# Performance work log

Measured on AMD Instinct MI355X. Metric: run time of the kernel, lower is better.

## Reference

```python
import jax, jax.numpy as jnp
import numpy as np

BETA = 0.25  # commitment weight (legacy=True branch)


def setup_inputs() -> dict:
    key = jax.random.key(0)
    k1, k2 = jax.random.split(key)
    B, C, H, W = 32, 256, 32, 32
    N_E, E_DIM = 1024, 256
    z = jax.random.normal(k1, (B, C, H, W), dtype=jnp.float32)
    # original init: uniform(-1/n_e, 1/n_e)
    emb = jax.random.uniform(k2, (N_E, E_DIM), dtype=jnp.float32,
                             minval=-1.0 / N_E, maxval=1.0 / N_E)
    return {"z": z, "emb": emb}


def reference(z, emb):
    B, C, H, W = z.shape
    sg = jax.lax.stop_gradient
    zt = jnp.transpose(z, (0, 2, 3, 1))            # b h w c
    zf = zt.reshape(-1, C)                          # (N, e_dim)
    # ||z||^2 + ||e||^2 - 2 z e^T  -> (N, n_e)
    d = (jnp.sum(zf * zf, axis=1, keepdims=True)
         + jnp.sum(emb * emb, axis=1)
         - 2.0 * jnp.einsum('nd,kd->nk', zf, emb))
    idx = jnp.argmin(d, axis=1)                     # (N,)
    z_q = emb[idx].reshape(zt.shape)                # b h w c
    # legacy=True loss
    loss = (jnp.mean((sg(z_q) - zt) ** 2)
            + BETA * jnp.mean((z_q - sg(zt)) ** 2))
    # straight-through estimator
    z_q_st = zt + sg(z_q - zt)
    z_q_out = jnp.transpose(z_q_st, (0, 3, 1, 2))   # b c h w
    z_indices = idx.reshape(B, 1, H, W)
    return z_q_out, loss, z_indices
```

## Files before the change

kernel.cpp:

```cpp
#include <hip/hip_runtime.h>


#define WS_B 0
#define WS_A 1024
#define WS_PV 132096
#define WS_E1 656384
#define WS_E2 787456
#define WS_LIST 918528
#define WS_CNT 951296
#define WS_Z1T 951304
#define WS_FUSED_BYTES ((size_t)(WS_Z1T + 8388608) * 4)

#define DDIM 256
#define LOSS_OFF 8388608
#define IDX_OFF 8388609
#define Z2T_OFF 8388608
#define REFINE_THR 8e-5f

typedef __attribute__((ext_vector_type(8))) short bf16x8;
typedef __attribute__((ext_vector_type(4))) float f32x4;
typedef __attribute__((ext_vector_type(8))) ushort u16x8;

__device__ __forceinline__ ushort bf16_rne(float x) {
  unsigned u = __float_as_uint(x);
  return (ushort)((u + 0x7FFFu + ((u >> 16) & 1u)) >> 16);
}
__device__ __forceinline__ float bf16f(ushort h) {
  return __uint_as_float(((unsigned)h) << 16);
}
__device__ __forceinline__ void gld16(void* l, const void* g) {
  __builtin_amdgcn_global_load_lds(
      (const __attribute__((address_space(1))) unsigned int*)g,
      (__attribute__((address_space(3))) unsigned int*)l, 16, 0, 0);
}

__global__ __launch_bounds__(256) void k_prep(const float* __restrict__ z,
                                              const float* __restrict__ emb,
                                              ushort* __restrict__ zt,
                                              float* __restrict__ ws,
                                              float* __restrict__ out) {
  __shared__ float lt[64][132];
  __shared__ float sq[128];
  const int tid = threadIdx.x;
  if (blockIdx.x >= 1024) {
    const int k = (blockIdx.x - 1024) * 256 + tid;
    if (k == 0) { out[LOSS_OFF] = 0.0f; ((int*)ws)[WS_CNT] = 0; }
    const int ct = k >> 8, n = k & 255;
    const float* er = emb + k * DDIM;
    ushort* e1t = (ushort*)(ws + WS_E1);
    ushort* e2t = (ushort*)(ws + WS_E2);
    float bsum = 0.f;
    for (int s = 0; s < 8; ++s) {
#pragma unroll
      for (int kq = 0; kq < 4; ++kq) {
        const float4 v0 = *(const float4*)(er + s * 32 + kq * 8);
        const float4 v1 = *(const float4*)(er + s * 32 + kq * 8 + 4);
        const float v[8] = {v0.x, v0.y, v0.z, v0.w, v1.x, v1.y, v1.z, v1.w};
        u16x8 h, l;
#pragma unroll
        for (int j = 0; j < 8; ++j) {
          bsum = fmaf(v[j], v[j], bsum);
          h[j] = bf16_rne(v[j]);
          l[j] = bf16_rne(v[j] - bf16f(h[j]));
        }
        const int off = ct * 65536 + s * 8192 + kq * 2048 + n * 8;
        *(u16x8*)(e1t + off) = h;
        *(u16x8*)(e2t + off) = l;
      }
    }
    ws[WS_B + k] = bsum;
    return;
  }
  const int rt = blockIdx.x >> 2;
  const int qp = blockIdx.x & 3;
  const int b = rt >> 3;
  const int hw0 = (rt & 7) << 7;
  ushort* z1t = zt;
  ushort* z2t = zt + Z2T_OFF;
  const int m = tid & 127, half = tid >> 7;
  const int lc = tid >> 2, lq = tid & 3;
  float as[4] = {0.f, 0.f, 0.f, 0.f};
  {
    const float* src = z + b * 262144 + ((qp << 6) + lc) * 1024 + hw0 + (lq << 5);
#pragma unroll
    for (int i = 0; i < 8; ++i)
      *(float4*)&lt[lc][(lq << 5) + (i << 2)] = *(const float4*)(src + (i << 2));
    __syncthreads();
    const int s = (qp << 1) + half;
#pragma unroll
    for (int kq = 0; kq < 4; ++kq) {
      u16x8 h, l;
#pragma unroll
      for (int j = 0; j < 8; ++j) {
        const float v = lt[(half << 5) + (kq << 3) + j][m];
        as[j & 3] = fmaf(v, v, as[j & 3]);
        h[j] = bf16_rne(v);
        l[j] = bf16_rne(v - bf16f(h[j]));
      }
      const int off = rt * 32768 + ((s << 2) + kq) * 1024 + (m << 3);
      *(u16x8*)(z1t + off) = h;
      *(u16x8*)(z2t + off) = l;
    }
    __syncthreads();
  }
  const float asum = (as[0] + as[1]) + (as[2] + as[3]);
  if (half) sq[m] = asum;
  __syncthreads();
  if (!half) ws[WS_A + qp * 32768 + rt * 128 + m] = asum + sq[m];
}

__global__ __launch_bounds__(512, 4) void k_score(const ushort* __restrict__ zt,
                                                  const float* __restrict__ emb,
                                                  float* out,
                                                  float* __restrict__ ws,
                                                  int fused) {
  __shared__ __align__(16) char smem[33312];
  ushort* zl = (ushort*)smem;
  float* Bs = (float*)(smem + 16384);
  float* pvs = (float*)(smem + 20480);
  float* sm2 = (float*)(smem + 33024);
  int* idxs = (int*)(smem + 33056);
  const int tid = threadIdx.x;
  const int bid = blockIdx.x;
  const int rt = ((bid >> 4) << 3) | (bid & 7);
  const int mh = ((bid >> 3) & 1) << 6;
  const int row0 = (rt << 7) + mh;
  const ushort* z1t = zt;
  const ushort* z2t = zt + Z2T_OFF;
  const ushort* e1t = (const ushort*)(ws + WS_E1);
  const ushort* e2t = (const ushort*)(ws + WS_E2);
  const int w = tid >> 6, L = tid & 63;
  const int l15 = L & 15, kq = L >> 4;
  const int wr = w >> 2, wc = w & 3;

  Bs[tid] = ws[WS_B + tid];
  Bs[tid + 512] = ws[WS_B + tid + 512];
  float Av[2][4];
#pragma unroll
  for (int mi = 0; mi < 2; ++mi) {
    const int base = row0 + (wr << 5) + (mi << 4) + (kq << 2);
    const float4 a0 = *(const float4*)(ws + WS_A + base);
    const float4 a1 = *(const float4*)(ws + WS_A + 32768 + base);
    const float4 a2 = *(const float4*)(ws + WS_A + 65536 + base);
    const float4 a3 = *(const float4*)(ws + WS_A + 98304 + base);
    Av[mi][0] = (a0.x + a1.x) + (a2.x + a3.x);
    Av[mi][1] = (a0.y + a1.y) + (a2.y + a3.y);
    Av[mi][2] = (a0.z + a1.z) + (a2.z + a3.z);
    Av[mi][3] = (a0.w + a1.w) + (a2.w + a3.w);
  }
  asm volatile("s_waitcnt vmcnt(0)" ::: "memory");
  __builtin_amdgcn_sched_barrier(0);
  __syncthreads();

  const ushort* zsrc = (w < 4 ? z1t : z2t) + rt * 32768 + ((w & 3) << 10)
                       + (mh << 3) + (L << 3);
  ushort* zdst0 = zl + ((w & 3) << 9) + ((w >> 2) << 11);
  auto stage = [&](int q, int bf) {
    gld16(zdst0 + (bf << 12), zsrc + ((q & 7) << 12));
  };
  const int ebase_th = (kq << 11) + (((wc << 6) + l15) << 3);

  f32x4 acc[2][4];
  float v1[2][4], v2[2][4];
  int i1[2][4];
#pragma unroll
  for (int mi = 0; mi < 2; ++mi)
#pragma unroll
    for (int r = 0; r < 4; ++r) {
      acc[mi][r] = (f32x4){0.f, 0.f, 0.f, 0.f};
      v1[mi][r] = 3.0e38f; v2[mi][r] = 3.0e38f; i1[mi][r] = 0;
    }

  stage(0, 0);
  stage(1, 1);

  auto body = [&](int q, int cur, bool last) {
    if (!last) asm volatile("s_waitcnt vmcnt(1)" ::: "memory");
    else       asm volatile("s_waitcnt vmcnt(0)" ::: "memory");
    __builtin_amdgcn_sched_barrier(0);
    __builtin_amdgcn_s_barrier();
    __builtin_amdgcn_sched_barrier(0);
    const ushort* lb = zl + (cur << 12);
    bf16x8 a1[2], a2[2], b1[4], b2[4];
#pragma unroll
    for (int mi = 0; mi < 2; ++mi) {
      const int off = (kq << 9) + (((wr << 5) + (mi << 4) + l15) << 3);
      a1[mi] = *(const bf16x8*)&lb[off];
      a2[mi] = *(const bf16x8*)&lb[2048 + off];
    }
    asm volatile("s_waitcnt lgkmcnt(0)" ::: "memory");
    __builtin_amdgcn_sched_barrier(0);
    __builtin_amdgcn_s_barrier();
    __builtin_amdgcn_sched_barrier(0);
    {
      const int ct = q >> 3, s = q & 7;
      const ushort* e1p = e1t + (ct << 16) + (s << 13) + ebase_th;
      const ushort* e2p = e2t + (ct << 16) + (s << 13) + ebase_th;
#pragma unroll
      for (int nj = 0; nj < 4; ++nj) {
        b1[nj] = *(const bf16x8*)(e1p + (nj << 7));
        b2[nj] = *(const bf16x8*)(e2p + (nj << 7));
      }
    }
    if (q < 30) stage(q + 2, cur);
    __builtin_amdgcn_s_setprio(1);
#pragma unroll
    for (int mi = 0; mi < 2; ++mi)
#pragma unroll
      for (int nj = 0; nj < 4; ++nj) {
        acc[mi][nj] = __builtin_amdgcn_mfma_f32_16x16x32_bf16(a2[mi], b1[nj], acc[mi][nj], 0, 0, 0);
        acc[mi][nj] = __builtin_amdgcn_mfma_f32_16x16x32_bf16(a1[mi], b2[nj], acc[mi][nj], 0, 0, 0);
        acc[mi][nj] = __builtin_amdgcn_mfma_f32_16x16x32_bf16(a1[mi], b1[nj], acc[mi][nj], 0, 0, 0);
      }
    __builtin_amdgcn_s_setprio(0);
    if ((q & 7) == 7) {
      const int ct = q >> 3;
      float bb[4];
#pragma unroll
      for (int nj = 0; nj < 4; ++nj)
        bb[nj] = Bs[(ct << 8) + (wc << 6) + (nj << 4) + l15];
      float cm[2][4];
#pragma unroll
      for (int mi = 0; mi < 2; ++mi)
#pragma unroll
        for (int r = 0; r < 4; ++r) cm[mi][r] = 3.0e38f;
#pragma unroll
      for (int mi = 0; mi < 2; ++mi)
#pragma unroll
        for (int nj = 0; nj < 4; ++nj) {
          const int kg = (ct << 8) + (wc << 6) + (nj << 4) + l15;
#pragma unroll
          for (int r = 0; r < 4; ++r) {
            const float sc = fmaf(-2.0f, acc[mi][nj][r], Av[mi][r] + bb[nj]);
            if (sc < v1[mi][r]) { v2[mi][r] = v1[mi][r]; v1[mi][r] = sc; i1[mi][r] = kg; }
            else if (sc < v2[mi][r]) v2[mi][r] = sc;
            cm[mi][r] = fminf(cm[mi][r], sc);
          }
          acc[mi][nj] = (f32x4){0.f, 0.f, 0.f, 0.f};
        }
#pragma unroll
      for (int mi = 0; mi < 2; ++mi)
#pragma unroll
        for (int r = 0; r < 4; ++r) {
          float cv = cm[mi][r];
#pragma unroll
          for (int o = 1; o < 16; o <<= 1) cv = fminf(cv, __shfl_xor(cv, o));
          if (l15 == 0) {
            const int rowl = (wr << 5) + (mi << 4) + (kq << 2) + r;
            pvs[((ct << 2) | wc) * 64 + rowl] = cv;
          }
        }
    }
  };

  for (int q = 0; q < 31; ++q) body(q, q & 1, false);
  body(31, 1, true);

#pragma unroll
  for (int mi = 0; mi < 2; ++mi)
#pragma unroll
    for (int r = 0; r < 4; ++r) {
      float a = v1[mi][r], bb = v2[mi][r];
      int ii = i1[mi][r];
#pragma unroll
      for (int o = 1; o < 16; o <<= 1) {
        const float oa = __shfl_xor(a, o);
        const float ob = __shfl_xor(bb, o);
        const int oi = __shfl_xor(ii, o);
        bb = fminf(fminf(bb, ob), fmaxf(a, oa));
        if (oa < a || (oa == a && oi < ii)) { a = oa; ii = oi; }
      }
      v1[mi][r] = a; v2[mi][r] = bb; i1[mi][r] = ii;
    }

  __syncthreads();
  for (int i = tid; i < 1024; i += 512) {
    const int c = i >> 6, rl = i & 63;
    ws[WS_PV + (c << 15) + row0 + rl] = pvs[i];
  }
  float* red = (float*)smem;
  if (l15 == 0) {
#pragma unroll
    for (int mi = 0; mi < 2; ++mi)
#pragma unroll
      for (int r = 0; r < 4; ++r) {
        const int rl = (wr << 5) + (mi << 4) + (kq << 2) + r;
        const int b3 = (wc * 64 + rl) * 3;
        red[b3] = v1[mi][r];
        red[b3 + 1] = v2[mi][r];
        red[b3 + 2] = (float)i1[mi][r];
      }
  }
  __syncthreads();
  float losss = 0.f;
  if (tid < 64) {
    float fv1 = 3.0e38f, fv2 = 3.0e38f;
    int fi = 0;
#pragma unroll
    for (int c = 0; c < 4; ++c) {
      const int b3 = (c * 64 + tid) * 3;
      const float a1 = red[b3], a2 = red[b3 + 1];
      const int ai = (int)red[b3 + 2];
      if (a1 < fv1 || (a1 == fv1 && ai < fi)) { fv2 = fminf(fv1, a2); fv1 = a1; fi = ai; }
      else fv2 = fminf(fv2, a1);
    }
    const int row = row0 + tid;
    out[IDX_OFF + row] = (float)fi;
    idxs[tid] = fi;
    if (fv2 - fv1 < REFINE_THR) {
      const int slot = atomicAdd((int*)ws + WS_CNT, 1);
      ((int*)ws)[WS_LIST + slot] = row;
    }
    losss = fv1;
  }
#pragma unroll
  for (int o = 32; o; o >>= 1) losss += __shfl_down(losss, o);
  if ((tid & 63) == 0) sm2[tid >> 6] = losss;
  __syncthreads();
  if (tid == 0) {
    float t = 0.f;
#pragma unroll
    for (int i = 0; i < 8; ++i) t += sm2[i];
    atomicAdd(out + LOSS_OFF, t * (1.25f / 8388608.0f));
  }

  if (fused) {
    float* lt2 = (float*)smem;
    const int b = row0 >> 10;
    const int hw0 = row0 & 1023;
    for (int ch = 0; ch < 2; ++ch) {
      __syncthreads();
      {
        const int r = tid >> 3, seg = tid & 7;
        const float* er = emb + idxs[r] * DDIM + (ch << 7);
        float* dst = lt2 + r * 129;
#pragma unroll
        for (int i = 0; i < 4; ++i) {
          const int c = (seg << 2) + (i << 5);
          const float4 v = *(const float4*)(er + c);
          dst[c] = v.x; dst[c + 1] = v.y; dst[c + 2] = v.z; dst[c + 3] = v.w;
        }
      }
      __syncthreads();
      {
        const int c = tid >> 2;
        const int r0 = (tid & 3) << 4;
        float* dsto = out + b * 262144 + ((ch << 7) + c) * 1024 + hw0 + r0;
#pragma unroll
        for (int i = 0; i < 16; i += 4) {
          float4 v;
          v.x = lt2[(r0 + i + 0) * 129 + c];
          v.y = lt2[(r0 + i + 1) * 129 + c];
          v.z = lt2[(r0 + i + 2) * 129 + c];
          v.w = lt2[(r0 + i + 3) * 129 + c];
          *(float4*)(dsto + i) = v;
        }
      }
    }
  }
}

__global__ __launch_bounds__(256) void k_refine(const float* __restrict__ z,
                                                const float* __restrict__ emb,
                                                const float* __restrict__ ws,
                                                float* __restrict__ out,
                                                int fused) {
  __shared__ float zs[4][256];
  const int tid = threadIdx.x;
  const int w = tid >> 6, L = tid & 63;
  const int wg = blockIdx.x * 4 + w;
  const int cnt = ((const int*)ws)[WS_CNT];
  for (int e = wg; e < cnt; e += 1024) {
    const int row = ((const int*)ws)[WS_LIST + e];
    const int b = row >> 10, hw = row & 1023;
#pragma unroll
    for (int q = 0; q < 4; ++q)
      zs[w][(q << 6) + L] = z[b * 262144 + (((q << 6) + L) << 10) + hw];
    asm volatile("s_waitcnt lgkmcnt(0)" ::: "memory");
    float v1c = (L < 16) ? ws[WS_PV + (L << 15) + row] : 3.0e38f;
    float v1 = v1c;
#pragma unroll
    for (int o = 1; o < 64; o <<= 1) v1 = fminf(v1, __shfl_xor(v1, o));
    const float A = (ws[WS_A + row] + ws[WS_A + 32768 + row]) +
                    (ws[WS_A + 65536 + row] + ws[WS_A + 98304 + row]);
    float bv = 3.0e38f;
    int bk = 0;
    for (int tc = 0; tc < 16; ++tc) {
      const float bc = __shfl(v1c, tc);
      if (bc <= v1 + REFINE_THR) {
        const int k = (tc << 6) + L;
        const float* er = emb + k * DDIM;
        float s = 0.f;
        for (int d = 0; d < DDIM; ++d) s = fmaf(zs[w][d], er[d], s);
        const float sc = fmaf(-2.0f, s, A + ws[WS_B + k]);
        if (sc < bv) { bv = sc; bk = k; }
      }
    }
#pragma unroll
    for (int o = 1; o < 64; o <<= 1) {
      const float ov = __shfl_xor(bv, o);
      const int ok = __shfl_xor(bk, o);
      if (ov < bv || (ov == bv && ok < bk)) { bv = ov; bk = ok; }
    }
    if (L == 0) out[IDX_OFF + row] = (float)bk;
    if (fused) {
#pragma unroll
      for (int ci = 0; ci < 4; ++ci) {
        const int c = (ci << 6) + L;
        out[b * 262144 + c * 1024 + hw] = emb[bk * DDIM + c];
      }
    }
  }
}

__global__ __launch_bounds__(256) void k_gather(const float* __restrict__ emb,
                                                float* __restrict__ out) {
  const int tid = threadIdx.x;
  const int e0 = (blockIdx.x * 256 + tid) * 16;
  const int b = e0 >> 18;
  const int c = (e0 >> 10) & 255;
  const int n0 = (b << 10) + (e0 & 1023);
#pragma unroll
  for (int g = 0; g < 4; ++g) {
    float q[4];
#pragma unroll
    for (int j = 0; j < 4; ++j) {
      const int id = (int)(out[IDX_OFF + n0 + g * 4 + j] + 0.5f);
      q[j] = emb[id * DDIM + c];
    }
    const float4 qv = {q[0], q[1], q[2], q[3]};
    *(float4*)(out + e0 + g * 4) = qv;
  }
}

extern "C" void kernel_launch(void* const* d_in, const int* in_sizes, int n_in,
                              void* d_out, int out_size, void* d_ws, size_t ws_size,
                              hipStream_t stream) {
  const float* z = (const float*)d_in[0];
  const float* emb = (const float*)d_in[1];
  float* out = (float*)d_out;
  float* ws = (float*)d_ws;
  const int fused = (ws_size >= WS_FUSED_BYTES) ? 1 : 0;
  ushort* zt = fused ? (ushort*)(ws + WS_Z1T) : (ushort*)out;

  k_prep<<<1028, 256, 0, stream>>>(z, emb, zt, ws, out);
  k_score<<<512, 512, 0, stream>>>(zt, emb, out, ws, fused);
  k_refine<<<256, 256, 0, stream>>>(z, emb, ws, out, fused);
  if (!fused) k_gather<<<2048, 256, 0, stream>>>(emb, out);
}
```

Before: 123.6 us.

## Process two K-steps per barrier pair with doubled LDS staging buffers

Restructures the scoring main loop so each iteration stages and consumes two 4K-element z chunks instead of one, halving the number of barrier/waitcnt synchronisation points per tile. LDS staging grows from two to two double-size buffers, and the fold step is factored into a helper called after the second substep. This raises LDS use per block (about 41 KB), which may reduce occupancy at four blocks of 512 threads per CU, and adds register pressure from the extra fragment set.

```diff
diff --git a/kernel.cpp b/kernel.cpp
--- a/kernel.cpp
+++ b/kernel.cpp
@@ -114,12 +114,12 @@
                                                   float* out,
                                                   float* __restrict__ ws,
                                                   int fused) {
-  __shared__ __align__(16) char smem[33312];
+  __shared__ __align__(16) char smem[41248];
   ushort* zl = (ushort*)smem;
-  float* Bs = (float*)(smem + 16384);
-  float* pvs = (float*)(smem + 20480);
-  float* sm2 = (float*)(smem + 33024);
-  int* idxs = (int*)(smem + 33056);
+  float* Bs = (float*)(smem + 32768);
+  float* pvs = (float*)(smem + 36864);
+  float* sm2 = (float*)(smem + 40960);
+  int* idxs = (int*)(smem + 40992);
   const int tid = threadIdx.x;
   const int bid = blockIdx.x;
   const int rt = ((bid >> 4) << 3) | (bid & 7);
@@ -155,8 +155,10 @@
   const ushort* zsrc = (w < 4 ? z1t : z2t) + rt * 32768 + ((w & 3) << 10)
                        + (mh << 3) + (L << 3);
   ushort* zdst0 = zl + ((w & 3) << 9) + ((w >> 2) << 11);
-  auto stage = [&](int q, int bf) {
-    gld16(zdst0 + (bf << 12), zsrc + ((q & 7) << 12));
+  auto stage2 = [&](int S, int bf) {
+#pragma unroll
+    for (int j = 0; j < 2; ++j)
+      gld16(zdst0 + (bf << 13) + (j << 12), zsrc + ((((S << 1) + j) & 7) << 12));
   };
   const int ebase_th = (kq << 11) + (((wc << 6) + l15) << 3);
 
@@ -171,38 +173,112 @@
       v1[mi][r] = 3.0e38f; v2[mi][r] = 3.0e38f; i1[mi][r] = 0;
     }
 
-  stage(0, 0);
-  stage(1, 1);
-
-  auto body = [&](int q, int cur, bool last) {
-    if (!last) asm volatile("s_waitcnt vmcnt(1)" ::: "memory");
-    else       asm volatile("s_waitcnt vmcnt(0)" ::: "memory");
-    __builtin_amdgcn_sched_barrier(0);
-    __builtin_amdgcn_s_barrier();
-    __builtin_amdgcn_sched_barrier(0);
-    const ushort* lb = zl + (cur << 12);
-    bf16x8 a1[2], a2[2], b1[4], b2[4];
+  stage2(0, 0);
+  stage2(1, 1);
+
+  auto substep = [&](int q, const ushort* lb) {
+    bf16x8 b1[4], b2[4], a1[2], a2[2];
+    {
+      const int ct = q >> 3, s = q & 7;
+      const ushort* e1p = e1t + (ct << 16) + (s << 13) + ebase_th;
+      const ushort* e2p = e2t + (ct << 16) + (s << 13) + ebase_th;
+#pragma unroll
+      for (int nj = 0; nj < 4; ++nj) {
+        b1[nj] = *(const bf16x8*)(e1p + (nj << 7));
+        b2[nj] = *(const bf16x8*)(e2p + (nj << 7));
+      }
+    }
 #pragma unroll
     for (int mi = 0; mi < 2; ++mi) {
       const int off = (kq << 9) + (((wr << 5) + (mi << 4) + l15) << 3);
       a1[mi] = *(const bf16x8*)&lb[off];
       a2[mi] = *(const bf16x8*)&lb[2048 + off];
     }
+    __builtin_amdgcn_s_setprio(1);
+#pragma unroll
+    for (int mi = 0; mi < 2; ++mi)
+#pragma unroll
+      for (int nj = 0; nj < 4; ++nj) {
+        acc[mi][nj] = __builtin_amdgcn_mfma_f32_16x16x32_bf16(a2[mi], b1[nj], acc[mi][nj], 0, 0, 0);
+        acc[mi][nj] = __builtin_amdgcn_mfma_f32_16x16x32_bf16(a1[mi], b2[nj], acc[mi][nj], 0, 0, 0);
+        acc[mi][nj] = __builtin_amdgcn_mfma_f32_16x16x32_bf16(a1[mi], b1[nj], acc[mi][nj], 0, 0, 0);
+      }
+    __builtin_amdgcn_s_setprio(0);
+  };
+  auto substep_loads = [&](int q, const ushort* lb, bf16x8 b1[4], bf16x8 b2[4],
+                           bf16x8 a1[2], bf16x8 a2[2]) {
+    const int ct = q >> 3, s = q & 7;
+    const ushort* e1p = e1t + (ct << 16) + (s << 13) + ebase_th;
+    const ushort* e2p = e2t + (ct << 16) + (s << 13) + ebase_th;
+#pragma unroll
+    for (int nj = 0; nj < 4; ++nj) {
+      b1[nj] = *(const bf16x8*)(e1p + (nj << 7));
+      b2[nj] = *(const bf16x8*)(e2p + (nj << 7));
+    }
+#pragma unroll
+    for (int mi = 0; mi < 2; ++mi) {
+      const int off = (kq << 9) + (((wr << 5) + (mi << 4) + l15) << 3);
+      a1[mi] = *(const bf16x8*)&lb[off];
+      a2[mi] = *(const bf16x8*)&lb[2048 + off];
+    }
+  };
+
+  auto fold = [&](int ct) {
+    float bb[4];
+#pragma unroll
+    for (int nj = 0; nj < 4; ++nj)
+      bb[nj] = Bs[(ct << 8) + (wc << 6) + (nj << 4) + l15];
+    float cm[2][4];
+#pragma unroll
+    for (int mi = 0; mi < 2; ++mi)
+#pragma unroll
+      for (int r = 0; r < 4; ++r) cm[mi][r] = 3.0e38f;
+#pragma unroll
+    for (int mi = 0; mi < 2; ++mi)
+#pragma unroll
+      for (int nj = 0; nj < 4; ++nj) {
+        const int kg = (ct << 8) + (wc << 6) + (nj << 4) + l15;
+#pragma unroll
+        for (int r = 0; r < 4; ++r) {
+          const float sc = fmaf(-2.0f, acc[mi][nj][r], Av[mi][r] + bb[nj]);
+          if (sc < v1[mi][r]) { v2[mi][r] = v1[mi][r]; v1[mi][r] = sc; i1[mi][r] = kg; }
+          else if (sc < v2[mi][r]) v2[mi][r] = sc;
+          cm[mi][r] = fminf(cm[mi][r], sc);
+        }
+        acc[mi][nj] = (f32x4){0.f, 0.f, 0.f, 0.f};
+      }
+#pragma unroll
+    for (int mi = 0; mi < 2; ++mi)
+#pragma unroll
+      for (int r = 0; r < 4; ++r) {
+        float cv = cm[mi][r];
+#pragma unroll
+        for (int o = 1; o < 16; o <<= 1) cv = fminf(cv, __shfl_xor(cv, o));
+        if (l15 == 0) {
+          const int rowl = (wr << 5) + (mi << 4) + (kq << 2) + r;
+          pvs[((ct << 2) | wc) * 64 + rowl] = cv;
+        }
+      }
+  };
+
+  for (int S = 0; S < 16; ++S) {
+    const int cur = S & 1;
+    const int q0 = S << 1, q1 = q0 + 1;
+    if (S < 15) asm volatile("s_waitcnt vmcnt(2)" ::: "memory");
+    else        asm volatile("s_waitcnt vmcnt(0)" ::: "memory");
+    __builtin_amdgcn_sched_barrier(0);
+    __builtin_amdgcn_s_barrier();
+    __builtin_amdgcn_sched_barrier(0);
+    const ushort* lb0 = zl + (cur << 13);
+    const ushort* lb1 = lb0 + 4096;
+    substep(q0, lb0);
+    bf16x8 b1[4], b2[4], a1[2], a2[2];
+    substep_loads(q1, lb1, b1, b2, a1, a2);
     asm volatile("s_waitcnt lgkmcnt(0)" ::: "memory");
     __builtin_amdgcn_sched_barrier(0);
     __builtin_amdgcn_s_barrier();
     __builtin_amdgcn_sched_barrier(0);
-    {
-      const int ct = q >> 3, s = q & 7;
-      const ushort* e1p = e1t + (ct << 16) + (s << 13) + ebase_th;
-      const ushort* e2p = e2t + (ct << 16) + (s << 13) + ebase_th;
-#pragma unroll
-      for (int nj = 0; nj < 4; ++nj) {
-        b1[nj] = *(const bf16x8*)(e1p + (nj << 7));
-        b2[nj] = *(const bf16x8*)(e2p + (nj << 7));
-      }
-    }
-    if (q < 30) stage(q + 2, cur);
+    if (S < 14) stage2(S + 2, cur);
     __builtin_amdgcn_s_setprio(1);
 #pragma unroll
     for (int mi = 0; mi < 2; ++mi)
@@ -213,48 +289,8 @@
         acc[mi][nj] = __builtin_amdgcn_mfma_f32_16x16x32_bf16(a1[mi], b1[nj], acc[mi][nj], 0, 0, 0);
       }
     __builtin_amdgcn_s_setprio(0);
-    if ((q & 7) == 7) {
-      const int ct = q >> 3;
-      float bb[4];
-#pragma unroll
-      for (int nj = 0; nj < 4; ++nj)
-        bb[nj] = Bs[(ct << 8) + (wc << 6) + (nj << 4) + l15];
-      float cm[2][4];
-#pragma unroll
-      for (int mi = 0; mi < 2; ++mi)
-#pragma unroll
-        for (int r = 0; r < 4; ++r) cm[mi][r] = 3.0e38f;
-#pragma unroll
-      for (int mi = 0; mi < 2; ++mi)
-#pragma unroll
-        for (int nj = 0; nj < 4; ++nj) {
-          const int kg = (ct << 8) + (wc << 6) + (nj << 4) + l15;
-#pragma unroll
-          for (int r = 0; r < 4; ++r) {
-            const float sc = fmaf(-2.0f, acc[mi][nj][r], Av[mi][r] + bb[nj]);
-            if (sc < v1[mi][r]) { v2[mi][r] = v1[mi][r]; v1[mi][r] = sc; i1[mi][r] = kg; }
-            else if (sc < v2[mi][r]) v2[mi][r] = sc;
-            cm[mi][r] = fminf(cm[mi][r], sc);
-          }
-          acc[mi][nj] = (f32x4){0.f, 0.f, 0.f, 0.f};
-        }
-#pragma unroll
-      for (int mi = 0; mi < 2; ++mi)
-#pragma unroll
-        for (int r = 0; r < 4; ++r) {
-          float cv = cm[mi][r];
-#pragma unroll
-          for (int o = 1; o < 16; o <<= 1) cv = fminf(cv, __shfl_xor(cv, o));
-          if (l15 == 0) {
-            const int rowl = (wr << 5) + (mi << 4) + (kq << 2) + r;
-            pvs[((ct << 2) | wc) * 64 + rowl] = cv;
-          }
-        }
-    }
-  };
-
-  for (int q = 0; q < 31; ++q) body(q, q & 1, false);
-  body(31, 1, true);
+    if ((q1 & 7) == 7) fold(q1 >> 3);
+  }
 
 #pragma unroll
   for (int mi = 0; mi < 2; ++mi)
```

After: 125.7 us. About the same (+1.7%).
